# Performance work log

Measured on AMD Instinct MI355X. Metric: run time of the kernel, lower is better.

## Reference

```python
import jax, jax.numpy as jnp
import numpy as np

# graph structure constants (uniform graphs => simple coloring / masks all-true)
G, NV, EPG, LEPG = 128, 32, 64, 256          # graphs, nodes/graph, g-edges/graph, lg-edges/graph
NG, NLG, ELG, K = G * NV, G * EPG, G * LEPG, EPG  # K = n_colors = lg-nodes per graph
H, HF, T, L, NC, FIN, FE, NB = 32, 128, 8, 4, 12, 16, 16, 4  # hidden, hidden_final, towers, layers, classes, node feats, edge feats, basis

_FLOATS = ('x_g','edge_attr_g','x_lg','edge_attr_lg','W_enc','b_enc','W_msg','b_msg','W_init','b_init','np_l1_w','np_l1_b','np_l2_w','np_l2_b','np_lin_w','np_lin_b','fe_l1_w','fe_l1_b','fe_l2_w','fe_l2_b','fe_lin_w','fe_lin_b','gd_w','gd_b','ga_w','ga_b','ld_w','ld_b','la_w','la_b','u1_w','u1_b','u2_w','u2_b','u3_w','u3_b','en_w','en_b','li_w','li_b','lj_w','lj_b','bn_g','bn_b','ac_w','ac_b','fl_w','fl_b')

def _lin(x, w, b):
    return x @ w + b

def _glin(x, w, b):
    # grouped (tower) linear: w [T, c, c], block-diagonal over channel groups
    t, ci, co = w.shape
    y = jnp.einsum('...tc,tcd->...td', x.reshape(x.shape[:-1] + (t, ci)), w)
    return y.reshape(x.shape[:-1] + (t * co,)) + b

def setup_inputs():
    rng = np.random.default_rng(0)
    off_n = np.arange(G)[:, None] * NV
    ei_g = np.stack([(rng.integers(0, NV, (G, EPG)) + off_n).ravel(),
                     (rng.integers(0, NV, (G, EPG)) + off_n).ravel()])
    off_e = np.arange(G)[:, None] * EPG
    ei_lg = np.stack([(rng.integers(0, EPG, (G, LEPG)) + off_e).ravel(),
                      (rng.integers(0, EPG, (G, LEPG)) + off_e).ravel()])
    keys = iter(jax.random.split(jax.random.key(0), 64))
    def nrm(shape, fan):
        return (jax.random.normal(next(keys), shape, dtype=jnp.float32) / np.float32(np.sqrt(fan)))
    z = lambda *s: jnp.zeros(s, jnp.float32)
    inp = {
        'x_g': nrm((NG, FIN), 1.0),
        'edge_attr_g': nrm((NLG, FE), 1.0),
        'x_lg': nrm((NLG, NB), 1.0),
        'edge_attr_lg': nrm((ELG, NB), 1.0),
        'W_enc': nrm((FIN, H), FIN), 'b_enc': z(H),
        'W_msg': nrm((2 * H + FE + NB, HF), 2 * H + FE + NB), 'b_msg': z(HF),
        'W_init': nrm((HF + 1, H), HF + 1), 'b_init': z(H),
        'np_l1_w': nrm((HF + 1, HF), HF + 1), 'np_l1_b': z(HF),
        'np_l2_w': nrm((HF + 1, HF), HF + 1), 'np_l2_b': z(HF),
        'np_lin_w': nrm((HF, HF), HF), 'np_lin_b': z(HF),
        'fe_l1_w': nrm((H, HF), H), 'fe_l1_b': z(HF),
        'fe_l2_w': nrm((H, HF), H), 'fe_l2_b': z(HF),
        'fe_lin_w': nrm((HF, HF), HF), 'fe_lin_b': z(HF),
        'gd_w': nrm((NB, NB), NB), 'gd_b': z(NB),
        'ga_w': nrm((NB, NB), NB), 'ga_b': z(NB),
        'ld_w': nrm((L, NB, H), NB), 'ld_b': z(L, H),
        'la_w': nrm((L, NB, H), NB), 'la_b': z(L, H),
        'u1_w': nrm((L, T, H // T, H // T), H // T), 'u1_b': z(L, H),
        'u2_w': nrm((L, T, H // T, H // T), H // T), 'u2_b': z(L, H),
        'u3_w': nrm((L, T, H // T, H // T), H // T), 'u3_b': z(L, H),
        'en_w': nrm((L, H, H), H), 'en_b': z(L, H),
        'li_w': nrm((L, T, H // T, H // T), H // T), 'li_b': z(L, H),
        'lj_w': nrm((L, T, H // T, H // T), H // T), 'lj_b': z(L, H),
        'bn_g': jnp.ones((L, H), jnp.float32), 'bn_b': z(L, H),
        'ac_w': nrm((HF, HF), HF), 'ac_b': z(HF),
        'fl_w': nrm((HF, NC), HF), 'fl_b': z(NC),
        'edge_index_g': jnp.asarray(ei_g, dtype=jnp.int32),
        'edge_index_lg': jnp.asarray(ei_lg, dtype=jnp.int32),
        'batch_g': jnp.asarray(np.repeat(np.arange(G), NV), dtype=jnp.int32),
    }
    return inp

def _forward(fl, edge_index_g, edge_index_lg, batch_g):
    p = dict(zip(_FLOATS, fl))
    h = _lin(p['x_g'], p['W_enc'], p['b_enc'])                                 # [NG, H]
    s, d = edge_index_g[0], edge_index_g[1]
    hm = _lin(jnp.concatenate([h[s], h[d], p['edge_attr_g'], p['x_lg']], -1),
              p['W_msg'], p['b_msg'])                                          # [NLG, HF]
    batch_lg = batch_g[s]                                                      # graph id per lg node
    coloring = jnp.arange(NLG, dtype=jnp.int32) - batch_lg * EPG               # local color in [0, K)
    onehot = (coloring[:, None] == jnp.arange(K)).astype(hm.dtype)             # [NLG, K]
    # map_x_to_u: one-hot identity channel + features on own color row
    u = jnp.concatenate([onehot[:, :, None], onehot[:, :, None] * hm[:, None, :]], 2)  # [NLG, K, HF+1]
    edge_glob = _lin(p['edge_attr_lg'], p['ga_w'], p['ga_b'])                  # [ELG, NB]
    dist_glob = _lin(p['x_lg'], p['gd_w'], p['gd_b'])                          # [NLG, NB]
    ls, ld = edge_index_lg[0], edge_index_lg[1]
    indeg = jax.ops.segment_sum(jnp.ones((ELG,), hm.dtype), ld, num_segments=NLG)
    avg_e = (jax.ops.segment_sum(indeg, batch_lg, num_segments=G) / EPG)[batch_lg]  # avg edges/graph per node
    idx = jnp.arange(NLG)
    nb = jnp.asarray(EPG, hm.dtype)                                            # lg nodes per graph

    def extract(u, w1, b1, w2, b2, lw, lb):
        # GraphExtractor: UtoGlobal (mean-over-colors pool + diagonal pool) + residual relu lin
        mean = jax.ops.segment_sum(u.sum(1) / nb, batch_lg, num_segments=G) / nb
        diag = jax.ops.segment_sum(u[idx, coloring], batch_lg, num_segments=G) / nb
        out = _lin(mean, w1, b1) + _lin(diag, w2, b2)
        return out + jax.nn.relu(_lin(out, lw, lb))

    out = extract(u, p['np_l1_w'], p['np_l1_b'], p['np_l2_w'], p['np_l2_b'], p['np_lin_w'], p['np_lin_b'])
    u = _lin(u, p['W_init'], p['b_init'])                                      # [NLG, K, H]
    for i in range(L):
        if i > 0:  # batch norm (training-mode stats over nodes x colors)
            m = u.mean((0, 1)); v = u.var((0, 1))
            u = (u - m) * jax.lax.rsqrt(v + 1e-5) * p['bn_g'][i] + p['bn_b'][i]
        dist_loc = _lin(dist_glob, p['ld_w'][i], p['ld_b'][i])                 # [NLG, H]
        edge_loc = _lin(edge_glob, p['la_w'][i], p['la_b'][i])                 # [ELG, H]
        # SMPLayer: UtoU message net (entrywise + color-mean + diagonal terms, towered)
        um = (_glin(u, p['u1_w'][i], p['u1_b'][i])
              + _glin(u.sum(1) / nb, p['u2_w'][i], p['u2_b'][i])[:, None, :]
              + _glin(u[idx, coloring], p['u3_w'][i], p['u3_b'][i])[:, None, :])
        um = um * dist_loc[:, None, :]                                         # distance-basis filter
        ui = _glin(um, p['li_w'][i], p['li_b'][i])
        uj = _glin(um, p['lj_w'][i], p['lj_b'][i])
        ef = _lin(edge_loc, p['en_w'][i], p['en_b'][i])[:, None, :]
        msg = um[ls] + jax.nn.relu(ui[ld] + uj[ls] + ef)                       # [ELG, K, H]
        u = jax.ops.segment_sum(msg, ld, num_segments=NLG) / avg_e[:, None, None] + u
        out = out + extract(u, p['fe_l1_w'], p['fe_l1_b'], p['fe_l2_w'], p['fe_l2_b'], p['fe_lin_w'], p['fe_lin_b']) / L
    out = jax.nn.relu(_lin(out, p['ac_w'], p['ac_b'])) + out
    return _lin(out, p['fl_w'], p['fl_b'])                                     # [G, NC]

def reference(x_g, edge_attr_g, x_lg, edge_attr_lg, W_enc, b_enc, W_msg, b_msg, W_init, b_init, np_l1_w, np_l1_b, np_l2_w, np_l2_b, np_lin_w, np_lin_b, fe_l1_w, fe_l1_b, fe_l2_w, fe_l2_b, fe_lin_w, fe_lin_b, gd_w, gd_b, ga_w, ga_b, ld_w, ld_b, la_w, la_b, u1_w, u1_b, u2_w, u2_b, u3_w, u3_b, en_w, en_b, li_w, li_b, lj_w, lj_b, bn_g, bn_b, ac_w, ac_b, fl_w, fl_b, edge_index_g, edge_index_lg, batch_g):
    args = dict(locals())
    fl = tuple(args[n] for n in _FLOATS)
    return _forward(fl, edge_index_g, edge_index_lg, batch_g)
```

## Files before the change

### kernel.cpp

```cpp
#include <hip/hip_runtime.h>

#define G_    128
#define NV_   32
#define EPG_  64
#define LEPG_ 256
#define NG_   (G_*NV_)
#define NLG_  (G_*EPG_)
#define ELG_  (G_*LEPG_)
#define K_    64
#define H_    32
#define HF_   128
#define L_    4
#define NC_   12
#define FIN_  16
#define FE_   16
#define NB_   4
#define TILE_ (K_*H_)

__global__ void k_init(float* bna) {
    int t = threadIdx.x;
    if (t < 256) bna[t] = 0.f;
}

__global__ __launch_bounds__(256) void k_pre(
    const float* __restrict__ xg, const float* __restrict__ Wenc,
    const float* __restrict__ benc,
    const float* __restrict__ ealg, const float* __restrict__ gaw,
    const float* __restrict__ gab,
    const float* __restrict__ xlg, const float* __restrict__ gdw,
    const float* __restrict__ gdb,
    float* __restrict__ h, float* __restrict__ eglob, float* __restrict__ dglob)
{
    int bid = blockIdx.x, t = threadIdx.x;
    if (bid < 512) {
        int gid = bid*256 + t; int nn = gid>>5, ch = gid&31;
        float s = benc[ch];
#pragma unroll
        for (int f = 0; f < FIN_; ++f) s += xg[nn*FIN_+f]*Wenc[f*H_+ch];
        h[gid] = s;
    } else {
        int gid = (bid-512)*256 + t;
        if (gid < ELG_*4) {
            int e = gid>>2, k = gid&3;
            float s = gab[k];
#pragma unroll
            for (int j = 0; j < 4; ++j) s += ealg[e*4+j]*gaw[j*4+k];
            eglob[gid] = s;
        } else {
            int gid2 = gid - ELG_*4;
            int nn = gid2>>2, k = gid2&3;
            float s = gdb[k];
#pragma unroll
            for (int j = 0; j < 4; ++j) s += xlg[nn*4+j]*gdw[j*4+k];
            dglob[gid2] = s;
        }
    }
}

__global__ __launch_bounds__(256) void k_p12(
    const float* __restrict__ h, const float* __restrict__ Wm,
    float* __restrict__ p1, float* __restrict__ p2) {
    int bid = blockIdx.x, t = threadIdx.x;
    int n = bid*2 + (t>>7), o = t&127;
    const float* hn = h + n*32;
    float a = 0.f, b = 0.f;
#pragma unroll
    for (int k = 0; k < 32; ++k) {
        float hv = hn[k];
        a += hv * Wm[k*HF_ + o];
        b += hv * Wm[(32+k)*HF_ + o];
    }
    p1[n*HF_ + o] = a; p2[n*HF_ + o] = b;
}

__global__ __launch_bounds__(256) void k_q34(
    const float* __restrict__ eag, const float* __restrict__ xlg,
    const float* __restrict__ Wm, const float* __restrict__ bm,
    float* __restrict__ q34) {
    int bid = blockIdx.x, t = threadIdx.x;
    int e = bid*2 + (t>>7), o = t&127;
    float s = bm[o];
#pragma unroll
    for (int k = 0; k < 16; ++k) s += eag[e*16+k] * Wm[(64+k)*HF_ + o];
#pragma unroll
    for (int k = 0; k < 4; ++k)  s += xlg[e*4+k]  * Wm[(80+k)*HF_ + o];
    q34[e*HF_ + o] = s;
}

__global__ __launch_bounds__(256) void k_msg2(
    const float* __restrict__ p1, const float* __restrict__ p2,
    const float* __restrict__ q34, const int* __restrict__ sidx,
    const int* __restrict__ didx, float* __restrict__ hm) {
    int idx = blockIdx.x*256 + threadIdx.x;
    int e = idx >> 5, o4 = idx & 31;
    int s = sidx[e], d = didx[e];
    float4 a = ((const float4*)p1)[s*32 + o4];
    float4 b = ((const float4*)p2)[d*32 + o4];
    float4 q = ((const float4*)q34)[e*32 + o4];
    ((float4*)hm)[idx] = make_float4(a.x+b.x+q.x, a.y+b.y+q.y, a.z+b.z+q.z, a.w+b.w+q.w);
}

__global__ __launch_bounds__(128) void k_out0(
    const float* __restrict__ hm, const float* __restrict__ l1w,
    const float* __restrict__ l1b, const float* __restrict__ l2w,
    const float* __restrict__ l2b, const float* __restrict__ lnw,
    const float* __restrict__ lnb, float* __restrict__ out_acc) {
    __shared__ float mh[128], o1[128];
    int g = blockIdx.x, t = threadIdx.x;
    float s = 0.f;
    for (int k = 0; k < 64; ++k) s += hm[(g*64+k)*HF_ + t];
    mh[t] = s * (1.f/64.f);
    __syncthreads();
    float o = l1b[t] + l2b[t] + (l1w[t]*(1.f/64.f) + l2w[t]);
    for (int k = 0; k < 128; ++k)
        o += mh[k] * (l1w[(1+k)*HF_ + t]*(1.f/64.f) + l2w[(1+k)*HF_ + t]);
    o1[t] = o;
    __syncthreads();
    float r = lnb[t];
    for (int k = 0; k < 128; ++k) r += o1[k] * lnw[k*HF_ + t];
    out_acc[g*HF_ + t] = o + (r > 0.f ? r : 0.f);
}

__global__ __launch_bounds__(256) void k_rv(
    const float* __restrict__ hm, const float* __restrict__ Wi,
    const float* __restrict__ bi, float* __restrict__ rv,
    float* __restrict__ cs, float* __restrict__ ds) {
    int bid = blockIdx.x, t = threadIdx.x;
    int n = bid*8 + (t>>5), ch = t&31;
    float s = Wi[ch];
    for (int f = 0; f < HF_; ++f) s += hm[n*HF_ + f] * Wi[(1+f)*H_ + ch];
    rv[n*32 + ch] = s;
    cs[n*32 + ch] = 64.f*bi[ch] + s;
    ds[n*32 + ch] = bi[ch] + s;
}

__global__ __launch_bounds__(256) void k_u0w(
    const float* __restrict__ rv, const float* __restrict__ bi,
    float* __restrict__ u0) {
    int bid = blockIdx.x, t = threadIdx.x;
    int c4 = t & 7;
    float4 b4 = ((const float4*)bi)[c4];
#pragma unroll
    for (int k = 0; k < 8; ++k) {
        int lin = bid*2048 + k*256 + t;
        int n = lin >> 9, c = (lin >> 3) & 63;
        float4 v = b4;
        if (c == (n & 63)) {
            float4 r = ((const float4*)rv)[n*8 + c4];
            v.x += r.x; v.y += r.y; v.z += r.z; v.w += r.w;
        }
        ((float4*)u0)[lin] = v;
    }
}

__global__ __launch_bounds__(256) void k_csr(
    const int* __restrict__ ls, const int* __restrict__ ld,
    int* __restrict__ offsg, int* __restrict__ csrp) {
    __shared__ int cnt[64], offs[65], cur[64];
    int g = blockIdx.x, t = threadIdx.x;
    if (t < 64) cnt[t] = 0;
    __syncthreads();
    int d = 0, sl = 0;
    d = ld[g*256 + t] & 63;
    sl = ls[g*256 + t] & 63;
    atomicAdd(&cnt[d], 1);
    __syncthreads();
    if (t == 0) {
        int a = 0;
        for (int i = 0; i < 64; ++i) { offs[i] = a; a += cnt[i]; }
        offs[64] = a;
    }
    __syncthreads();
    if (t < 64) { cur[t] = offs[t]; offsg[g*65 + t] = offs[t]; }
    if (t == 0) offsg[g*65 + 64] = offs[64];
    __syncthreads();
    int p = atomicAdd(&cur[d], 1);
    csrp[g*256 + p] = (t << 6) | sl;
}

__global__ __launch_bounds__(256) void k_dlef(
    const float* __restrict__ dgl, const float* __restrict__ egl,
    const float* __restrict__ ldw, const float* __restrict__ ldb,
    const float* __restrict__ law, const float* __restrict__ lab,
    const float* __restrict__ enw, const float* __restrict__ enb,
    float* __restrict__ dlb, float* __restrict__ efb) {
    int bid = blockIdx.x, t = threadIdx.x;
    if (bid < 4096) {
        int gid = bid*256 + t;
        int l = gid >> 18, rem = gid & ((1<<18)-1);
        int n = rem >> 5, ch = rem & 31;
        float s = ldb[l*32 + ch];
#pragma unroll
        for (int j = 0; j < 4; ++j) s += dgl[n*4+j] * ldw[l*128 + j*32 + ch];
        dlb[gid] = s;
    } else {
        __shared__ float el[8][32];
        int p = (bid - 4096)*8 + (t >> 5);
        int ch = t & 31;
        int l = p >> 15, e = p & 32767;
        float s = lab[l*32 + ch];
#pragma unroll
        for (int j = 0; j < 4; ++j) s += egl[e*4+j] * law[l*128 + j*32 + ch];
        el[t>>5][ch] = s;
        __syncthreads();
        float o = enb[l*32 + ch];
        for (int k = 0; k < 32; ++k) o += el[t>>5][k] * enw[l*1024 + k*32 + ch];
        efb[(size_t)l*ELG_*32 + e*32 + ch] = o;
    }
}

__global__ __launch_bounds__(256) void k_gtdl(
    const float* __restrict__ cs, const float* __restrict__ ds,
    const float* __restrict__ bnaP, const float* __restrict__ bng,
    const float* __restrict__ bnb, int lay,
    const float* __restrict__ u1w, const float* __restrict__ u2w,
    const float* __restrict__ u3w, const float* __restrict__ u1b,
    const float* __restrict__ u2b, const float* __restrict__ u3b,
    const float* __restrict__ dl_l, float* __restrict__ gtb) {
    int idx = blockIdx.x*256 + threadIdx.x;
    int n = idx >> 5, ch = idx & 31;
    int chi = ch & 3, twb = ch & ~3;
    float gt = u1b[ch] + u2b[ch] + u3b[ch];
#pragma unroll
    for (int j = 0; j < 4; ++j) {
        int bj = twb + j;
        float s_ = 1.f, sh_ = 0.f;
        if (lay > 0) {
            float m = bnaP[bj] * (1.f/524288.f);
            float v = bnaP[32+bj] * (1.f/524288.f) - m*m;
            s_ = bng[bj] * rsqrtf(v + 1e-5f);
            sh_ = bnb[bj] - m*s_;
        }
        float csF = s_*cs[n*32 + bj] + 64.f*sh_;
        float dgF = s_*ds[n*32 + bj] + sh_;
        gt += csF*(1.f/64.f)*u2w[bj*4 + chi] + dgF*u3w[bj*4 + chi]
            + sh_*u1w[bj*4 + chi];
    }
    gtb[idx] = gt * dl_l[idx];
}

#define PROC_NODE(ACC, UI, JE)                                              \
  for (; j < (JE); ++j) {                                                   \
    int jn = j + 2; jn = jn < 255 ? jn : 255;                               \
    int pkN = ep[jn];                                                       \
    float4 efN = *(const float4*)(ef_l + (((size_t)((g<<8)+(pkN>>6)))<<5) + chb); \
    int src = pkA & 63;                                                     \
    float4 u4 = *(float4*)&um[src*128 + coff];                              \
    float r0 = UI.x + efA.x + blj4[0] + u4.x*wj[0] + u4.y*wj[4] + u4.z*wj[8] + u4.w*wj[12]; \
    float r1 = UI.y + efA.y + blj4[1] + u4.x*wj[1] + u4.y*wj[5] + u4.z*wj[9] + u4.w*wj[13]; \
    float r2 = UI.z + efA.z + blj4[2] + u4.x*wj[2] + u4.y*wj[6] + u4.z*wj[10] + u4.w*wj[14]; \
    float r3 = UI.w + efA.w + blj4[3] + u4.x*wj[3] + u4.y*wj[7] + u4.z*wj[11] + u4.w*wj[15]; \
    ACC.x += u4.x + (r0>0.f?r0:0.f);                                        \
    ACC.y += u4.y + (r1>0.f?r1:0.f);                                        \
    ACC.z += u4.z + (r2>0.f?r2:0.f);                                        \
    ACC.w += u4.w + (r3>0.f?r3:0.f);                                        \
    pkA = pkB; efA = efB; pkB = pkN; efB = efN;                             \
  }

#define UM_NODE(I, UIOUT, DL, GT)                                           \
  {                                                                         \
    int nl = nq*4 + I;                                                      \
    float4 uv = *(float4*)&us[nl*128 + coff];                               \
    float m0 = (uv.x*w1f[0]+uv.y*w1f[4]+uv.z*w1f[8] +uv.w*w1f[12])*DL.x + GT.x; \
    float m1 = (uv.x*w1f[1]+uv.y*w1f[5]+uv.z*w1f[9] +uv.w*w1f[13])*DL.y + GT.y; \
    float m2 = (uv.x*w1f[2]+uv.y*w1f[6]+uv.z*w1f[10]+uv.w*w1f[14])*DL.z + GT.z; \
    float m3 = (uv.x*w1f[3]+uv.y*w1f[7]+uv.z*w1f[11]+uv.w*w1f[15])*DL.w + GT.w; \
    *(float4*)&um[nl*128 + coff] = make_float4(m0,m1,m2,m3);                \
    UIOUT.x = bli4[0] + m0*wi[0] + m1*wi[4] + m2*wi[8]  + m3*wi[12];        \
    UIOUT.y = bli4[1] + m0*wi[1] + m1*wi[5] + m2*wi[9]  + m3*wi[13];        \
    UIOUT.z = bli4[2] + m0*wi[2] + m1*wi[6] + m2*wi[10] + m3*wi[14];        \
    UIOUT.w = bli4[3] + m0*wi[3] + m1*wi[7] + m2*wi[11] + m3*wi[15];        \
  }

#define UN_NODE(I, ACC)                                                     \
  {                                                                         \
    float4 uo4 = *(float4*)&us[(nq*4+I)*128 + coff];                        \
    float4 un4;                                                             \
    un4.x = ACC.x*0.25f + sc4[0]*uo4.x + sh4[0];                            \
    un4.y = ACC.y*0.25f + sc4[1]*uo4.y + sh4[1];                            \
    un4.z = ACC.z*0.25f + sc4[2]*uo4.z + sh4[2];                            \
    un4.w = ACC.w*0.25f + sc4[3]*uo4.w + sh4[3];                            \
    *(float4*)(u_out + (((size_t)(n0g+I))<<11) + (ck<<7) + coff) = un4;     \
    if (nq == ck && c == I)                                                 \
        *(float4*)&dsb[(((size_t)(n0g+I))<<5) + chb] = un4;                 \
    float cx=un4.x, cy=un4.y, cz=un4.z, cw=un4.w;                           \
    float qx=cx*cx, qy=cy*cy, qz=cz*cz, qw=cw*cw;                           \
    cx+=__shfl_xor(cx,8);  cy+=__shfl_xor(cy,8);  cz+=__shfl_xor(cz,8);  cw+=__shfl_xor(cw,8); \
    qx+=__shfl_xor(qx,8);  qy+=__shfl_xor(qy,8);  qz+=__shfl_xor(qz,8);  qw+=__shfl_xor(qw,8); \
    cx+=__shfl_xor(cx,16); cy+=__shfl_xor(cy,16); cz+=__shfl_xor(cz,16); cw+=__shfl_xor(cw,16); \
    qx+=__shfl_xor(qx,16); qy+=__shfl_xor(qy,16); qz+=__shfl_xor(qz,16); qw+=__shfl_xor(qw,16); \
    if (c == 0) {                                                           \
        *(float4*)&pcs[(((size_t)(ck*NLG_ + n0g + I))<<5) + chb] = make_float4(cx,cy,cz,cw); \
        *(float4*)&pss[(((size_t)(ck*NLG_ + n0g + I))<<5) + chb] = make_float4(qx,qy,qz,qw); \
    }                                                                       \
  }

__global__ __launch_bounds__(512, 4) void k_layer(
    const float* __restrict__ u_in, float* __restrict__ u_out,
    const int* __restrict__ offsg, const int* __restrict__ csrp,
    const float* __restrict__ bnaP, const float* __restrict__ bng,
    const float* __restrict__ bnb, int lay,
    const float* __restrict__ u1w,
    const float* __restrict__ liw, const float* __restrict__ lib,
    const float* __restrict__ ljw, const float* __restrict__ ljb,
    const float* __restrict__ dl_l, const float* __restrict__ gtb,
    const float* __restrict__ ef_l,
    float* __restrict__ pcs, float* __restrict__ pss, float* __restrict__ dsb)
{
    __shared__ float us[64*128];
    __shared__ float um[64*128];
    __shared__ int ep[256];
    __shared__ int offs[65];

    const int bid = blockIdx.x, t = threadIdx.x;
    const int g  = ((bid >> 7) << 3) | (bid & 7);
    const int ck = (bid >> 3) & 15;
    const int tw = t & 7, c = (t >> 3) & 3, nq = t >> 5;
    const int chb = tw * 4;
    const int coff = c*32 + chb;
    const int n0g = g*64 + nq*4;

    if (t < 256) ep[t] = csrp[g*256 + t];
    else if (t < 256 + 65) offs[t - 256] = offsg[g*65 + (t - 256)];

    {
        const float* ub = u_in + ((size_t)g << 17) + (ck << 7);
#pragma unroll
        for (int r = 0; r < 4; ++r) {
            int lin = r*2048 + t*4;
            int nl = lin >> 7, off = lin & 127;
            float4 v = *(const float4*)(ub + ((size_t)nl << 11) + off);
            *(float4*)&us[lin] = v;
        }
    }

    float4 dl0 = *(const float4*)(dl_l + (((size_t)(n0g+0))<<5) + chb);
    float4 dl1 = *(const float4*)(dl_l + (((size_t)(n0g+1))<<5) + chb);
    float4 dl2 = *(const float4*)(dl_l + (((size_t)(n0g+2))<<5) + chb);
    float4 dl3 = *(const float4*)(dl_l + (((size_t)(n0g+3))<<5) + chb);
    float4 gt0 = *(const float4*)(gtb + (((size_t)(n0g+0))<<5) + chb);
    float4 gt1 = *(const float4*)(gtb + (((size_t)(n0g+1))<<5) + chb);
    float4 gt2 = *(const float4*)(gtb + (((size_t)(n0g+2))<<5) + chb);
    float4 gt3 = *(const float4*)(gtb + (((size_t)(n0g+3))<<5) + chb);

    float sc4[4], sh4[4];
    if (lay > 0) {
#pragma unroll
        for (int j = 0; j < 4; ++j) {
            int bj = chb + j;
            float m = bnaP[bj] * (1.f/524288.f);
            float v = bnaP[32+bj] * (1.f/524288.f) - m*m;
            float s_ = bng[bj] * rsqrtf(v + 1e-5f);
            sc4[j] = s_; sh4[j] = bnb[bj] - m*s_;
        }
    } else {
#pragma unroll
        for (int j = 0; j < 4; ++j) { sc4[j] = 1.f; sh4[j] = 0.f; }
    }
    float w1f[16], wi[16], wj[16], bli4[4], blj4[4];
#pragma unroll
    for (int j = 0; j < 4; ++j)
#pragma unroll
        for (int d = 0; d < 4; ++d) {
            w1f[j*4+d] = u1w[(chb+j)*4 + d] * sc4[j];
            wi [j*4+d] = liw[(chb+j)*4 + d];
            wj [j*4+d] = ljw[(chb+j)*4 + d];
        }
#pragma unroll
    for (int d = 0; d < 4; ++d) { bli4[d] = lib[chb+d]; blj4[d] = ljb[chb+d]; }

    __syncthreads();

    float4 ui0, ui1, ui2, ui3;
    UM_NODE(0, ui0, dl0, gt0)
    UM_NODE(1, ui1, dl1, gt1)
    UM_NODE(2, ui2, dl2, gt2)
    UM_NODE(3, ui3, dl3, gt3)
    __syncthreads();

    float4 acc0 = make_float4(0,0,0,0), acc1 = acc0, acc2 = acc0, acc3 = acc0;
    int j = offs[nq*4];
    {
        int ja = j < 255 ? j : 255;
        int pkA = ep[ja];
        float4 efA = *(const float4*)(ef_l + (((size_t)((g<<8)+(pkA>>6)))<<5) + chb);
        int jb = (j+1) < 255 ? (j+1) : 255;
        int pkB = ep[jb];
        float4 efB = *(const float4*)(ef_l + (((size_t)((g<<8)+(pkB>>6)))<<5) + chb);
        int e1 = offs[nq*4+1], e2 = offs[nq*4+2], e3 = offs[nq*4+3], e4 = offs[nq*4+4];
        PROC_NODE(acc0, ui0, e1)
        PROC_NODE(acc1, ui1, e2)
        PROC_NODE(acc2, ui2, e3)
        PROC_NODE(acc3, ui3, e4)
    }

    UN_NODE(0, acc0)
    UN_NODE(1, acc1)
    UN_NODE(2, acc2)
    UN_NODE(3, acc3)
}

__global__ __launch_bounds__(256) void k_midx(
    const float* __restrict__ pcs, const float* __restrict__ pss,
    const float* __restrict__ dsb,
    const float* __restrict__ l1w, const float* __restrict__ l1b,
    const float* __restrict__ l2w, const float* __restrict__ l2b,
    const float* __restrict__ lnw, const float* __restrict__ lnb,
    float* __restrict__ csb, float* __restrict__ bna_i,
    float* __restrict__ out_acc, float scale)
{
    __shared__ float red[3*128];
    __shared__ float S[32], D[32], o1[128];
    int g = blockIdx.x, t = threadIdx.x;
    int ch = t & 31, ng = t >> 5;
    float pS = 0.f, pQ = 0.f, pD = 0.f;
#pragma unroll
    for (int k = 0; k < 8; ++k) {
        int n = g*64 + ng + 8*k;
        float cs_ = 0.f, ss_ = 0.f;
#pragma unroll
        for (int ckk = 0; ckk < 16; ++ckk) {
            cs_ += pcs[((size_t)ckk*NLG_ + n)*32 + ch];
            ss_ += pss[((size_t)ckk*NLG_ + n)*32 + ch];
        }
        csb[n*32 + ch] = cs_;
        pS += cs_; pQ += ss_;
        pD += dsb[n*32 + ch];
    }
    pS += __shfl_xor(pS, 32); pQ += __shfl_xor(pQ, 32); pD += __shfl_xor(pD, 32);
    int w = t >> 6;
    if ((t & 63) < 32) {
        red[w*32 + ch] = pS;
        red[128 + w*32 + ch] = pQ;
        red[256 + w*32 + ch] = pD;
    }
    __syncthreads();
    if (t < 32) {
        float S_ = 0.f, Q_ = 0.f, D_ = 0.f;
#pragma unroll
        for (int ww = 0; ww < 4; ++ww) {
            S_ += red[ww*32 + t]; Q_ += red[128 + ww*32 + t]; D_ += red[256 + ww*32 + t];
        }
        S[t] = S_; D[t] = D_;
        atomicAdd(&bna_i[t], S_);
        atomicAdd(&bna_i[32 + t], Q_);
    }
    __syncthreads();
    float o = 0.f;
    if (t < 128) {
        o = l1b[t] + l2b[t];
        for (int k = 0; k < 32; ++k)
            o += (S[k]*(1.f/4096.f))*l1w[k*HF_ + t] + (D[k]*(1.f/64.f))*l2w[k*HF_ + t];
        o1[t] = o;
    }
    __syncthreads();
    if (t < 128) {
        float r = lnb[t];
        for (int k = 0; k < 128; ++k) r += o1[k] * lnw[k*HF_ + t];
        out_acc[g*HF_ + t] += (o + (r > 0.f ? r : 0.f)) * scale;
    }
}

__global__ __launch_bounds__(128) void k_final(
    const float* __restrict__ out_acc, const float* __restrict__ acw,
    const float* __restrict__ acb, const float* __restrict__ flw,
    const float* __restrict__ flb, float* __restrict__ out) {
    __shared__ float t1[128];
    int g = blockIdx.x, t = threadIdx.x;
    float o = out_acc[g*HF_ + t];
    float r = acb[t];
    for (int k = 0; k < 128; ++k) r += out_acc[g*HF_ + k] * acw[k*HF_ + t];
    t1[t] = o + (r > 0.f ? r : 0.f);
    __syncthreads();
    if (t < NC_) {
        float s = flb[t];
        for (int k = 0; k < 128; ++k) s += t1[k] * flw[k*NC_ + t];
        out[g*NC_ + t] = s;
    }
}

extern "C" void kernel_launch(void* const* d_in, const int* in_sizes, int n_in,
                              void* d_out, int out_size, void* d_ws, size_t ws_size,
                              hipStream_t stream) {
    const float* x_g      = (const float*)d_in[0];
    const float* eag      = (const float*)d_in[1];
    const float* x_lg     = (const float*)d_in[2];
    const float* ealg     = (const float*)d_in[3];
    const float* W_enc    = (const float*)d_in[4];
    const float* b_enc    = (const float*)d_in[5];
    const float* W_msg    = (const float*)d_in[6];
    const float* b_msg    = (const float*)d_in[7];
    const float* W_init   = (const float*)d_in[8];
    const float* b_init   = (const float*)d_in[9];
    const float* np_l1_w  = (const float*)d_in[10];
    const float* np_l1_b  = (const float*)d_in[11];
    const float* np_l2_w  = (const float*)d_in[12];
    const float* np_l2_b  = (const float*)d_in[13];
    const float* np_lin_w = (const float*)d_in[14];
    const float* np_lin_b = (const float*)d_in[15];
    const float* fe_l1_w  = (const float*)d_in[16];
    const float* fe_l1_b  = (const float*)d_in[17];
    const float* fe_l2_w  = (const float*)d_in[18];
    const float* fe_l2_b  = (const float*)d_in[19];
    const float* fe_lin_w = (const float*)d_in[20];
    const float* fe_lin_b = (const float*)d_in[21];
    const float* gd_w     = (const float*)d_in[22];
    const float* gd_b     = (const float*)d_in[23];
    const float* ga_w     = (const float*)d_in[24];
    const float* ga_b     = (const float*)d_in[25];
    const float* ld_w     = (const float*)d_in[26];
    const float* ld_b     = (const float*)d_in[27];
    const float* la_w     = (const float*)d_in[28];
    const float* la_b     = (const float*)d_in[29];
    const float* u1_w     = (const float*)d_in[30];
    const float* u1_b     = (const float*)d_in[31];
    const float* u2_w     = (const float*)d_in[32];
    const float* u2_b     = (const float*)d_in[33];
    const float* u3_w     = (const float*)d_in[34];
    const float* u3_b     = (const float*)d_in[35];
    const float* en_w     = (const float*)d_in[36];
    const float* en_b     = (const float*)d_in[37];
    const float* li_w     = (const float*)d_in[38];
    const float* li_b     = (const float*)d_in[39];
    const float* lj_w     = (const float*)d_in[40];
    const float* lj_b     = (const float*)d_in[41];
    const float* bn_g     = (const float*)d_in[42];
    const float* bn_b     = (const float*)d_in[43];
    const float* ac_w     = (const float*)d_in[44];
    const float* ac_b     = (const float*)d_in[45];
    const float* fl_w     = (const float*)d_in[46];
    const float* fl_b     = (const float*)d_in[47];
    const int*   ei_g     = (const int*)d_in[48];
    const int*   ei_lg    = (const int*)d_in[49];

    const int* s_g  = ei_g;
    const int* d_g  = ei_g + NLG_;
    const int* ls   = ei_lg;
    const int* ldst = ei_lg + ELG_;

    float* ws = (float*)d_ws;
    size_t o = 0;
    float* ub0  = ws + o; o += (size_t)NLG_ * TILE_;
    float* ub1  = ws + o; o += (size_t)NLG_ * TILE_;
    float* hm   = ws + o; o += (size_t)NLG_ * HF_;
    float* hbuf = ws + o; o += (size_t)NG_ * H_;
    float* dgl  = ws + o; o += (size_t)NLG_ * NB_;
    float* egl  = ws + o; o += (size_t)ELG_ * NB_;
    float* p1b  = ws + o; o += (size_t)NG_ * HF_;
    float* p2b  = ws + o; o += (size_t)NG_ * HF_;
    float* q34b = ws + o; o += (size_t)NLG_ * HF_;
    float* rvb  = ws + o; o += (size_t)NLG_ * 32;
    float* csb  = ws + o; o += (size_t)NLG_ * 32;
    float* dsb  = ws + o; o += (size_t)NLG_ * 32;
    float* gtb  = ws + o; o += (size_t)NLG_ * 32;
    float* pcs  = ws + o; o += (size_t)16 * NLG_ * 32;
    float* pss  = ws + o; o += (size_t)16 * NLG_ * 32;
    float* oac  = ws + o; o += (size_t)G_ * HF_;
    float* bna  = ws + o; o += 256;
    float* dlb  = ws + o; o += (size_t)L_ * NLG_ * 32;
    float* efb  = ws + o; o += (size_t)L_ * ELG_ * 32;
    int*   offsg = (int*)(ws + o); o += G_ * 65;
    int*   csrp  = (int*)(ws + o); o += ELG_;

    k_init<<<1, 256, 0, stream>>>(bna);
    k_pre<<<1152, 256, 0, stream>>>(x_g, W_enc, b_enc, ealg, ga_w, ga_b,
                                    x_lg, gd_w, gd_b, hbuf, egl, dgl);
    k_p12<<<2048, 256, 0, stream>>>(hbuf, W_msg, p1b, p2b);
    k_q34<<<4096, 256, 0, stream>>>(eag, x_lg, W_msg, b_msg, q34b);
    k_msg2<<<1024, 256, 0, stream>>>(p1b, p2b, q34b, s_g, d_g, hm);
    k_dlef<<<4096 + 16384, 256, 0, stream>>>(dgl, egl, ld_w, ld_b, la_w, la_b,
                                             en_w, en_b, dlb, efb);
    k_out0<<<G_, 128, 0, stream>>>(hm, np_l1_w, np_l1_b, np_l2_w, np_l2_b,
                                   np_lin_w, np_lin_b, oac);
    k_rv<<<1024, 256, 0, stream>>>(hm, W_init, b_init, rvb, csb, dsb);
    k_u0w<<<2048, 256, 0, stream>>>(rvb, b_init, ub0);
    k_csr<<<G_, 256, 0, stream>>>(ls, ldst, offsg, csrp);
    k_gtdl<<<1024, 256, 0, stream>>>(csb, dsb, bna, bn_g, bn_b, 0,
                                     u1_w, u2_w, u3_w, u1_b, u2_b, u3_b,
                                     dlb, gtb);

    float* ubufs[2] = {ub0, ub1};
    for (int i = 0; i < L_; ++i) {
        const float* ui = ubufs[i & 1];
        float* uo = ubufs[(i + 1) & 1];
        k_layer<<<2048, 512, 0, stream>>>(
            ui, uo, offsg, csrp,
            (i > 0 ? bna + (i-1)*64 : bna), bn_g + i*32, bn_b + i*32, i,
            u1_w + i*128,
            li_w + i*128, li_b + i*32,
            lj_w + i*128, lj_b + i*32,
            dlb + (size_t)i*NLG_*32, gtb, efb + (size_t)i*ELG_*32,
            pcs, pss, dsb);
        k_midx<<<G_, 256, 0, stream>>>(
            pcs, pss, dsb,
            fe_l1_w, fe_l1_b, fe_l2_w, fe_l2_b, fe_lin_w, fe_lin_b,
            csb, bna + i*64, oac, 1.0f / (float)L_);
        if (i < L_ - 1)
            k_gtdl<<<1024, 256, 0, stream>>>(csb, dsb, bna + i*64,
                                             bn_g + (i+1)*32, bn_b + (i+1)*32, i+1,
                                             u1_w + (i+1)*128, u2_w + (i+1)*128,
                                             u3_w + (i+1)*128, u1_b + (i+1)*32,
                                             u2_b + (i+1)*32, u3_b + (i+1)*32,
                                             dlb + (size_t)(i+1)*NLG_*32, gtb);
    }
    k_final<<<G_, 128, 0, stream>>>(oac, ac_w, ac_b, fl_w, fl_b, (float*)d_out);
}
```

Before: 571.5 us.

## Merge preprocessing kernels, drop u shared staging, synthesize layer-0 u, fuse final head

```diff
diff --git a/kernel.cpp b/kernel.cpp
--- a/kernel.cpp
+++ b/kernel.cpp
@@ -17,176 +17,134 @@
 #define NB_   4
 #define TILE_ (K_*H_)
 
-__global__ void k_init(float* bna) {
-    int t = threadIdx.x;
-    if (t < 256) bna[t] = 0.f;
-}
-
-__global__ __launch_bounds__(256) void k_pre(
+__global__ __launch_bounds__(256) void kA(
     const float* __restrict__ xg, const float* __restrict__ Wenc,
     const float* __restrict__ benc,
     const float* __restrict__ ealg, const float* __restrict__ gaw,
     const float* __restrict__ gab,
     const float* __restrict__ xlg, const float* __restrict__ gdw,
     const float* __restrict__ gdb,
-    float* __restrict__ h, float* __restrict__ eglob, float* __restrict__ dglob)
+    const float* __restrict__ eag, const float* __restrict__ Wm,
+    const float* __restrict__ bm,
+    const float* __restrict__ h_unused,
+    const int* __restrict__ ls, const int* __restrict__ ldst,
+    float* __restrict__ h, float* __restrict__ eglob, float* __restrict__ dglob,
+    float* __restrict__ p1, float* __restrict__ p2, float* __restrict__ q34,
+    int* __restrict__ offsg, int* __restrict__ csrp, float* __restrict__ bna)
 {
+    __shared__ int cnt[64], offs[65], cur[64];
     int bid = blockIdx.x, t = threadIdx.x;
-    if (bid < 512) {
-        int gid = bid*256 + t; int nn = gid>>5, ch = gid&31;
-        float s = benc[ch];
-#pragma unroll
-        for (int f = 0; f < FIN_; ++f) s += xg[nn*FIN_+f]*Wenc[f*H_+ch];
-        h[gid] = s;
-    } else {
-        int gid = (bid-512)*256 + t;
-        if (gid < ELG_*4) {
-            int e = gid>>2, k = gid&3;
-            float s = gab[k];
-#pragma unroll
-            for (int j = 0; j < 4; ++j) s += ealg[e*4+j]*gaw[j*4+k];
-            eglob[gid] = s;
+    if (bid == 0) {
+        bna[t] = 0.f;
+        return;
+    }
+    if (bid < 1 + 1152) {
+        int lb = bid - 1;
+        if (lb < 512) {
+            int gid = lb*256 + t; int nn = gid>>5, ch = gid&31;
+            float s = benc[ch];
+#pragma unroll
+            for (int f = 0; f < FIN_; ++f) s += xg[nn*FIN_+f]*Wenc[f*H_+ch];
+            h[gid] = s;
         } else {
-            int gid2 = gid - ELG_*4;
-            int nn = gid2>>2, k = gid2&3;
-            float s = gdb[k];
-#pragma unroll
-            for (int j = 0; j < 4; ++j) s += xlg[nn*4+j]*gdw[j*4+k];
-            dglob[gid2] = s;
-        }
+            int gid = (lb-512)*256 + t;
+            if (gid < ELG_*4) {
+                int e = gid>>2, k = gid&3;
+                float s = gab[k];
+#pragma unroll
+                for (int j = 0; j < 4; ++j) s += ealg[e*4+j]*gaw[j*4+k];
+                eglob[gid] = s;
+            } else {
+                int gid2 = gid - ELG_*4;
+                int nn = gid2>>2, k = gid2&3;
+                float s = gdb[k];
+#pragma unroll
+                for (int j = 0; j < 4; ++j) s += xlg[nn*4+j]*gdw[j*4+k];
+                dglob[gid2] = s;
+            }
+        }
+        return;
+    }
+    if (bid < 1 + 1152 + 2048) {
+        int lb = bid - 1153;
+        int n = lb*2 + (t>>7), o = t&127;
+        const float* hn = h_unused + n*32;
+        (void)hn;
+        float hv[32];
+#pragma unroll
+        for (int k = 0; k < 32; ++k) {
+            float s = benc[k];
+#pragma unroll
+            for (int f = 0; f < FIN_; ++f) s += xg[n*FIN_+f]*Wenc[f*H_+k];
+            hv[k] = s;
+        }
+        float a = 0.f, b = 0.f;
+#pragma unroll
+        for (int k = 0; k < 32; ++k) {
+            a += hv[k] * Wm[k*HF_ + o];
+            b += hv[k] * Wm[(32+k)*HF_ + o];
+        }
+        p1[n*HF_ + o] = a; p2[n*HF_ + o] = b;
+        return;
+    }
+    if (bid < 1 + 1152 + 2048 + 4096) {
+        int lb = bid - 3201;
+        int e = lb*2 + (t>>7), o = t&127;
+        float s = bm[o];
+#pragma unroll
+        for (int k = 0; k < 16; ++k) s += eag[e*16+k] * Wm[(64+k)*HF_ + o];
+#pragma unroll
+        for (int k = 0; k < 4; ++k)  s += xlg[e*4+k]  * Wm[(80+k)*HF_ + o];
+        q34[e*HF_ + o] = s;
+        return;
+    }
+    {
+        int g = bid - 7297;
+        if (t < 64) cnt[t] = 0;
+        __syncthreads();
+        int d = ldst[g*256 + t] & 63;
+        int sl = ls[g*256 + t] & 63;
+        atomicAdd(&cnt[d], 1);
+        __syncthreads();
+        if (t == 0) {
+            int a = 0;
+            for (int i = 0; i < 64; ++i) { offs[i] = a; a += cnt[i]; }
+            offs[64] = a;
+        }
+        __syncthreads();
+        if (t < 64) { cur[t] = offs[t]; offsg[g*65 + t] = offs[t]; }
+        if (t == 0) offsg[g*65 + 64] = offs[64];
+        __syncthreads();
+        int p = atomicAdd(&cur[d], 1);
+        csrp[g*256 + p] = (t << 6) | sl;
     }
 }
 
-__global__ __launch_bounds__(256) void k_p12(
-    const float* __restrict__ h, const float* __restrict__ Wm,
-    float* __restrict__ p1, float* __restrict__ p2) {
-    int bid = blockIdx.x, t = threadIdx.x;
-    int n = bid*2 + (t>>7), o = t&127;
-    const float* hn = h + n*32;
-    float a = 0.f, b = 0.f;
-#pragma unroll
-    for (int k = 0; k < 32; ++k) {
-        float hv = hn[k];
-        a += hv * Wm[k*HF_ + o];
-        b += hv * Wm[(32+k)*HF_ + o];
-    }
-    p1[n*HF_ + o] = a; p2[n*HF_ + o] = b;
-}
-
-__global__ __launch_bounds__(256) void k_q34(
-    const float* __restrict__ eag, const float* __restrict__ xlg,
-    const float* __restrict__ Wm, const float* __restrict__ bm,
-    float* __restrict__ q34) {
-    int bid = blockIdx.x, t = threadIdx.x;
-    int e = bid*2 + (t>>7), o = t&127;
-    float s = bm[o];
-#pragma unroll
-    for (int k = 0; k < 16; ++k) s += eag[e*16+k] * Wm[(64+k)*HF_ + o];
-#pragma unroll
-    for (int k = 0; k < 4; ++k)  s += xlg[e*4+k]  * Wm[(80+k)*HF_ + o];
-    q34[e*HF_ + o] = s;
-}
-
-__global__ __launch_bounds__(256) void k_msg2(
+__global__ __launch_bounds__(256) void kB(
     const float* __restrict__ p1, const float* __restrict__ p2,
     const float* __restrict__ q34, const int* __restrict__ sidx,
-    const int* __restrict__ didx, float* __restrict__ hm) {
-    int idx = blockIdx.x*256 + threadIdx.x;
-    int e = idx >> 5, o4 = idx & 31;
-    int s = sidx[e], d = didx[e];
-    float4 a = ((const float4*)p1)[s*32 + o4];
-    float4 b = ((const float4*)p2)[d*32 + o4];
-    float4 q = ((const float4*)q34)[e*32 + o4];
-    ((float4*)hm)[idx] = make_float4(a.x+b.x+q.x, a.y+b.y+q.y, a.z+b.z+q.z, a.w+b.w+q.w);
-}
-
-__global__ __launch_bounds__(128) void k_out0(
-    const float* __restrict__ hm, const float* __restrict__ l1w,
-    const float* __restrict__ l1b, const float* __restrict__ l2w,
-    const float* __restrict__ l2b, const float* __restrict__ lnw,
-    const float* __restrict__ lnb, float* __restrict__ out_acc) {
-    __shared__ float mh[128], o1[128];
-    int g = blockIdx.x, t = threadIdx.x;
-    float s = 0.f;
-    for (int k = 0; k < 64; ++k) s += hm[(g*64+k)*HF_ + t];
-    mh[t] = s * (1.f/64.f);
-    __syncthreads();
-    float o = l1b[t] + l2b[t] + (l1w[t]*(1.f/64.f) + l2w[t]);
-    for (int k = 0; k < 128; ++k)
-        o += mh[k] * (l1w[(1+k)*HF_ + t]*(1.f/64.f) + l2w[(1+k)*HF_ + t]);
-    o1[t] = o;
-    __syncthreads();
-    float r = lnb[t];
-    for (int k = 0; k < 128; ++k) r += o1[k] * lnw[k*HF_ + t];
-    out_acc[g*HF_ + t] = o + (r > 0.f ? r : 0.f);
-}
-
-__global__ __launch_bounds__(256) void k_rv(
-    const float* __restrict__ hm, const float* __restrict__ Wi,
-    const float* __restrict__ bi, float* __restrict__ rv,
-    float* __restrict__ cs, float* __restrict__ ds) {
-    int bid = blockIdx.x, t = threadIdx.x;
-    int n = bid*8 + (t>>5), ch = t&31;
-    float s = Wi[ch];
-    for (int f = 0; f < HF_; ++f) s += hm[n*HF_ + f] * Wi[(1+f)*H_ + ch];
-    rv[n*32 + ch] = s;
-    cs[n*32 + ch] = 64.f*bi[ch] + s;
-    ds[n*32 + ch] = bi[ch] + s;
-}
-
-__global__ __launch_bounds__(256) void k_u0w(
-    const float* __restrict__ rv, const float* __restrict__ bi,
-    float* __restrict__ u0) {
-    int bid = blockIdx.x, t = threadIdx.x;
-    int c4 = t & 7;
-    float4 b4 = ((const float4*)bi)[c4];
-#pragma unroll
-    for (int k = 0; k < 8; ++k) {
-        int lin = bid*2048 + k*256 + t;
-        int n = lin >> 9, c = (lin >> 3) & 63;
-        float4 v = b4;
-        if (c == (n & 63)) {
-            float4 r = ((const float4*)rv)[n*8 + c4];
-            v.x += r.x; v.y += r.y; v.z += r.z; v.w += r.w;
-        }
-        ((float4*)u0)[lin] = v;
-    }
-}
-
-__global__ __launch_bounds__(256) void k_csr(
-    const int* __restrict__ ls, const int* __restrict__ ld,
-    int* __restrict__ offsg, int* __restrict__ csrp) {
-    __shared__ int cnt[64], offs[65], cur[64];
-    int g = blockIdx.x, t = threadIdx.x;
-    if (t < 64) cnt[t] = 0;
-    __syncthreads();
-    int d = 0, sl = 0;
-    d = ld[g*256 + t] & 63;
-    sl = ls[g*256 + t] & 63;
-    atomicAdd(&cnt[d], 1);
-    __syncthreads();
-    if (t == 0) {
-        int a = 0;
-        for (int i = 0; i < 64; ++i) { offs[i] = a; a += cnt[i]; }
-        offs[64] = a;
-    }
-    __syncthreads();
-    if (t < 64) { cur[t] = offs[t]; offsg[g*65 + t] = offs[t]; }
-    if (t == 0) offsg[g*65 + 64] = offs[64];
-    __syncthreads();
-    int p = atomicAdd(&cur[d], 1);
-    csrp[g*256 + p] = (t << 6) | sl;
-}
-
-__global__ __launch_bounds__(256) void k_dlef(
+    const int* __restrict__ didx, float* __restrict__ hm,
     const float* __restrict__ dgl, const float* __restrict__ egl,
     const float* __restrict__ ldw, const float* __restrict__ ldb,
     const float* __restrict__ law, const float* __restrict__ lab,
     const float* __restrict__ enw, const float* __restrict__ enb,
-    float* __restrict__ dlb, float* __restrict__ efb) {
+    float* __restrict__ dlb, float* __restrict__ efb)
+{
+    __shared__ float el[8][32];
     int bid = blockIdx.x, t = threadIdx.x;
-    if (bid < 4096) {
-        int gid = bid*256 + t;
+    if (bid < 1024) {
+        int idx = bid*256 + t;
+        int e = idx >> 5, o4 = idx & 31;
+        int s = sidx[e], d = didx[e];
+        float4 a = ((const float4*)p1)[s*32 + o4];
+        float4 b = ((const float4*)p2)[d*32 + o4];
+        float4 q = ((const float4*)q34)[e*32 + o4];
+        ((float4*)hm)[idx] = make_float4(a.x+b.x+q.x, a.y+b.y+q.y, a.z+b.z+q.z, a.w+b.w+q.w);
+        return;
+    }
+    int lb = bid - 1024;
+    if (lb < 4096) {
+        int gid = lb*256 + t;
         int l = gid >> 18, rem = gid & ((1<<18)-1);
         int n = rem >> 5, ch = rem & 31;
         float s = ldb[l*32 + ch];
@@ -194,8 +152,7 @@
         for (int j = 0; j < 4; ++j) s += dgl[n*4+j] * ldw[l*128 + j*32 + ch];
         dlb[gid] = s;
     } else {
-        __shared__ float el[8][32];
-        int p = (bid - 4096)*8 + (t >> 5);
+        int p = (lb - 4096)*8 + (t >> 5);
         int ch = t & 31;
         int l = p >> 15, e = p & 32767;
         float s = lab[l*32 + ch];
@@ -206,6 +163,48 @@
         float o = enb[l*32 + ch];
         for (int k = 0; k < 32; ++k) o += el[t>>5][k] * enw[l*1024 + k*32 + ch];
         efb[(size_t)l*ELG_*32 + e*32 + ch] = o;
+    }
+}
+
+__global__ __launch_bounds__(256) void kC(
+    const float* __restrict__ hm, const float* __restrict__ Wi,
+    const float* __restrict__ bi, float* __restrict__ rv,
+    float* __restrict__ cs, float* __restrict__ ds,
+    const float* __restrict__ l1w, const float* __restrict__ l1b,
+    const float* __restrict__ l2w, const float* __restrict__ l2b,
+    const float* __restrict__ lnw, const float* __restrict__ lnb,
+    float* __restrict__ out_acc)
+{
+    __shared__ float mh[128], o1[128];
+    int bid = blockIdx.x, t = threadIdx.x;
+    if (bid < 1024) {
+        int n = bid*8 + (t>>5), ch = t&31;
+        float s = Wi[ch];
+        for (int f = 0; f < HF_; ++f) s += hm[n*HF_ + f] * Wi[(1+f)*H_ + ch];
+        rv[n*32 + ch] = s;
+        cs[n*32 + ch] = 64.f*bi[ch] + s;
+        ds[n*32 + ch] = bi[ch] + s;
+        return;
+    }
+    int g = bid - 1024;
+    if (t < 128) {
+        float s = 0.f;
+        for (int k = 0; k < 64; ++k) s += hm[(g*64+k)*HF_ + t];
+        mh[t] = s * (1.f/64.f);
+    }
+    __syncthreads();
+    float o = 0.f;
+    if (t < 128) {
+        o = l1b[t] + l2b[t] + (l1w[t]*(1.f/64.f) + l2w[t]);
+        for (int k = 0; k < 128; ++k)
+            o += mh[k] * (l1w[(1+k)*HF_ + t]*(1.f/64.f) + l2w[(1+k)*HF_ + t]);
+        o1[t] = o;
+    }
+    __syncthreads();
+    if (t < 128) {
+        float r = lnb[t];
+        for (int k = 0; k < 128; ++k) r += o1[k] * lnw[k*HF_ + t];
+        out_acc[g*HF_ + t] = o + (r > 0.f ? r : 0.f);
     }
 }
 
@@ -257,30 +256,28 @@
     pkA = pkB; efA = efB; pkB = pkN; efB = efN;                             \
   }
 
-#define UM_NODE(I, UIOUT, DL, GT)                                           \
+#define UM_NODE(I, UIOUT, UO, DL, GT)                                       \
   {                                                                         \
-    int nl = nq*4 + I;                                                      \
-    float4 uv = *(float4*)&us[nl*128 + coff];                               \
-    float m0 = (uv.x*w1f[0]+uv.y*w1f[4]+uv.z*w1f[8] +uv.w*w1f[12])*DL.x + GT.x; \
-    float m1 = (uv.x*w1f[1]+uv.y*w1f[5]+uv.z*w1f[9] +uv.w*w1f[13])*DL.y + GT.y; \
-    float m2 = (uv.x*w1f[2]+uv.y*w1f[6]+uv.z*w1f[10]+uv.w*w1f[14])*DL.z + GT.z; \
-    float m3 = (uv.x*w1f[3]+uv.y*w1f[7]+uv.z*w1f[11]+uv.w*w1f[15])*DL.w + GT.w; \
-    *(float4*)&um[nl*128 + coff] = make_float4(m0,m1,m2,m3);                \
+    float m0 = (UO.x*w1f[0]+UO.y*w1f[4]+UO.z*w1f[8] +UO.w*w1f[12])*DL.x + GT.x; \
+    float m1 = (UO.x*w1f[1]+UO.y*w1f[5]+UO.z*w1f[9] +UO.w*w1f[13])*DL.y + GT.y; \
+    float m2 = (UO.x*w1f[2]+UO.y*w1f[6]+UO.z*w1f[10]+UO.w*w1f[14])*DL.z + GT.z; \
+    float m3 = (UO.x*w1f[3]+UO.y*w1f[7]+UO.z*w1f[11]+UO.w*w1f[15])*DL.w + GT.w; \
+    *(float4*)&um[(nq*4+I)*128 + coff] = make_float4(m0,m1,m2,m3);          \
     UIOUT.x = bli4[0] + m0*wi[0] + m1*wi[4] + m2*wi[8]  + m3*wi[12];        \
     UIOUT.y = bli4[1] + m0*wi[1] + m1*wi[5] + m2*wi[9]  + m3*wi[13];        \
     UIOUT.z = bli4[2] + m0*wi[2] + m1*wi[6] + m2*wi[10] + m3*wi[14];        \
     UIOUT.w = bli4[3] + m0*wi[3] + m1*wi[7] + m2*wi[11] + m3*wi[15];        \
   }
 
-#define UN_NODE(I, ACC)                                                     \
+#define UN_NODE(I, ACC, UO)                                                 \
   {                                                                         \
-    float4 uo4 = *(float4*)&us[(nq*4+I)*128 + coff];                        \
     float4 un4;                                                             \
-    un4.x = ACC.x*0.25f + sc4[0]*uo4.x + sh4[0];                            \
-    un4.y = ACC.y*0.25f + sc4[1]*uo4.y + sh4[1];                            \
-    un4.z = ACC.z*0.25f + sc4[2]*uo4.z + sh4[2];                            \
-    un4.w = ACC.w*0.25f + sc4[3]*uo4.w + sh4[3];                            \
-    *(float4*)(u_out + (((size_t)(n0g+I))<<11) + (ck<<7) + coff) = un4;     \
+    un4.x = ACC.x*0.25f + sc4[0]*UO.x + sh4[0];                             \
+    un4.y = ACC.y*0.25f + sc4[1]*UO.y + sh4[1];                             \
+    un4.z = ACC.z*0.25f + sc4[2]*UO.z + sh4[2];                             \
+    un4.w = ACC.w*0.25f + sc4[3]*UO.w + sh4[3];                             \
+    if (!last)                                                              \
+        *(float4*)(u_out + (((size_t)(n0g+I))<<11) + (ck<<7) + coff) = un4; \
     if (nq == ck && c == I)                                                 \
         *(float4*)&dsb[(((size_t)(n0g+I))<<5) + chb] = un4;                 \
     float cx=un4.x, cy=un4.y, cz=un4.z, cw=un4.w;                           \
@@ -295,11 +292,12 @@
     }                                                                       \
   }
 
-__global__ __launch_bounds__(512, 4) void k_layer(
+__global__ __launch_bounds__(512, 6) void k_layer(
     const float* __restrict__ u_in, float* __restrict__ u_out,
     const int* __restrict__ offsg, const int* __restrict__ csrp,
     const float* __restrict__ bnaP, const float* __restrict__ bng,
-    const float* __restrict__ bnb, int lay,
+    const float* __restrict__ bnb, int lay, int last,
+    const float* __restrict__ rvb, const float* __restrict__ bi,
     const float* __restrict__ u1w,
     const float* __restrict__ liw, const float* __restrict__ lib,
     const float* __restrict__ ljw, const float* __restrict__ ljb,
@@ -307,7 +305,6 @@
     const float* __restrict__ ef_l,
     float* __restrict__ pcs, float* __restrict__ pss, float* __restrict__ dsb)
 {
-    __shared__ float us[64*128];
     __shared__ float um[64*128];
     __shared__ int ep[256];
     __shared__ int offs[65];
@@ -323,15 +320,23 @@
     if (t < 256) ep[t] = csrp[g*256 + t];
     else if (t < 256 + 65) offs[t - 256] = offsg[g*65 + (t - 256)];
 
-    {
-        const float* ub = u_in + ((size_t)g << 17) + (ck << 7);
-#pragma unroll
-        for (int r = 0; r < 4; ++r) {
-            int lin = r*2048 + t*4;
-            int nl = lin >> 7, off = lin & 127;
-            float4 v = *(const float4*)(ub + ((size_t)nl << 11) + off);
-            *(float4*)&us[lin] = v;
-        }
+    float4 uo0, uo1, uo2, uo3;
+    if (lay == 0) {
+        float4 b4 = *(const float4*)(bi + chb);
+        uo0 = b4; uo1 = b4; uo2 = b4; uo3 = b4;
+        if (nq == ck) {
+            float4 r = *(const float4*)(rvb + (size_t)(n0g + c)*32 + chb);
+            if      (c == 0) { uo0.x+=r.x; uo0.y+=r.y; uo0.z+=r.z; uo0.w+=r.w; }
+            else if (c == 1) { uo1.x+=r.x; uo1.y+=r.y; uo1.z+=r.z; uo1.w+=r.w; }
+            else if (c == 2) { uo2.x+=r.x; uo2.y+=r.y; uo2.z+=r.z; uo2.w+=r.w; }
+            else             { uo3.x+=r.x; uo3.y+=r.y; uo3.z+=r.z; uo3.w+=r.w; }
+        }
+    } else {
+        const float* ub = u_in + ((size_t)n0g << 11) + (ck << 7) + coff;
+        uo0 = *(const float4*)(ub);
+        uo1 = *(const float4*)(ub + 2048);
+        uo2 = *(const float4*)(ub + 4096);
+        uo3 = *(const float4*)(ub + 6144);
     }
 
     float4 dl0 = *(const float4*)(dl_l + (((size_t)(n0g+0))<<5) + chb);
@@ -346,36 +351,34 @@
     float sc4[4], sh4[4];
     if (lay > 0) {
 #pragma unroll
-        for (int j = 0; j < 4; ++j) {
-            int bj = chb + j;
+        for (int j2 = 0; j2 < 4; ++j2) {
+            int bj = chb + j2;
             float m = bnaP[bj] * (1.f/524288.f);
             float v = bnaP[32+bj] * (1.f/524288.f) - m*m;
             float s_ = bng[bj] * rsqrtf(v + 1e-5f);
-            sc4[j] = s_; sh4[j] = bnb[bj] - m*s_;
+            sc4[j2] = s_; sh4[j2] = bnb[bj] - m*s_;
         }
     } else {
 #pragma unroll
-        for (int j = 0; j < 4; ++j) { sc4[j] = 1.f; sh4[j] = 0.f; }
+        for (int j2 = 0; j2 < 4; ++j2) { sc4[j2] = 1.f; sh4[j2] = 0.f; }
     }
     float w1f[16], wi[16], wj[16], bli4[4], blj4[4];
 #pragma unroll
-    for (int j = 0; j < 4; ++j)
+    for (int j2 = 0; j2 < 4; ++j2)
 #pragma unroll
         for (int d = 0; d < 4; ++d) {
-            w1f[j*4+d] = u1w[(chb+j)*4 + d] * sc4[j];
-            wi [j*4+d] = liw[(chb+j)*4 + d];
-            wj [j*4+d] = ljw[(chb+j)*4 + d];
+            w1f[j2*4+d] = u1w[(chb+j2)*4 + d] * sc4[j2];
+            wi [j2*4+d] = liw[(chb+j2)*4 + d];
+            wj [j2*4+d] = ljw[(chb+j2)*4 + d];
         }
 #pragma unroll
     for (int d = 0; d < 4; ++d) { bli4[d] = lib[chb+d]; blj4[d] = ljb[chb+d]; }
 
-    __syncthreads();
-
     float4 ui0, ui1, ui2, ui3;
-    UM_NODE(0, ui0, dl0, gt0)
-    UM_NODE(1, ui1, dl1, gt1)
-    UM_NODE(2, ui2, dl2, gt2)
-    UM_NODE(3, ui3, dl3, gt3)
+    UM_NODE(0, ui0, uo0, dl0, gt0)
+    UM_NODE(1, ui1, uo1, dl1, gt1)
+    UM_NODE(2, ui2, uo2, dl2, gt2)
+    UM_NODE(3, ui3, uo3, dl3, gt3)
     __syncthreads();
 
     float4 acc0 = make_float4(0,0,0,0), acc1 = acc0, acc2 = acc0, acc3 = acc0;
@@ -394,10 +397,10 @@
         PROC_NODE(acc3, ui3, e4)
     }
 
-    UN_NODE(0, acc0)
-    UN_NODE(1, acc1)
-    UN_NODE(2, acc2)
-    UN_NODE(3, acc3)
+    UN_NODE(0, acc0, uo0)
+    UN_NODE(1, acc1, uo1)
+    UN_NODE(2, acc2, uo2)
+    UN_NODE(3, acc3, uo3)
 }
 
 __global__ __launch_bounds__(256) void k_midx(
@@ -407,10 +410,13 @@
     const float* __restrict__ l2w, const float* __restrict__ l2b,
     const float* __restrict__ lnw, const float* __restrict__ lnb,
     float* __restrict__ csb, float* __restrict__ bna_i,
-    float* __restrict__ out_acc, float scale)
+    float* __restrict__ out_acc, float scale,
+    int do_final, const float* __restrict__ acw, const float* __restrict__ acb,
+    const float* __restrict__ flw, const float* __restrict__ flb,
+    float* __restrict__ outp)
 {
     __shared__ float red[3*128];
-    __shared__ float S[32], D[32], o1[128];
+    __shared__ float S[32], D[32], o1[128], ov[128], t1[128];
     int g = blockIdx.x, t = threadIdx.x;
     int ch = t & 31, ng = t >> 5;
     float pS = 0.f, pQ = 0.f, pD = 0.f;
@@ -454,28 +460,27 @@
         o1[t] = o;
     }
     __syncthreads();
+    float newv = 0.f;
     if (t < 128) {
         float r = lnb[t];
         for (int k = 0; k < 128; ++k) r += o1[k] * lnw[k*HF_ + t];
-        out_acc[g*HF_ + t] += (o + (r > 0.f ? r : 0.f)) * scale;
-    }
-}
-
-__global__ __launch_bounds__(128) void k_final(
-    const float* __restrict__ out_acc, const float* __restrict__ acw,
-    const float* __restrict__ acb, const float* __restrict__ flw,
-    const float* __restrict__ flb, float* __restrict__ out) {
-    __shared__ float t1[128];
-    int g = blockIdx.x, t = threadIdx.x;
-    float o = out_acc[g*HF_ + t];
-    float r = acb[t];
-    for (int k = 0; k < 128; ++k) r += out_acc[g*HF_ + k] * acw[k*HF_ + t];
-    t1[t] = o + (r > 0.f ? r : 0.f);
-    __syncthreads();
-    if (t < NC_) {
-        float s = flb[t];
-        for (int k = 0; k < 128; ++k) s += t1[k] * flw[k*NC_ + t];
-        out[g*NC_ + t] = s;
+        newv = out_acc[g*HF_ + t] + (o + (r > 0.f ? r : 0.f)) * scale;
+        out_acc[g*HF_ + t] = newv;
+        ov[t] = newv;
+    }
+    if (do_final) {
+        __syncthreads();
+        if (t < 128) {
+            float r2 = acb[t];
+            for (int k = 0; k < 128; ++k) r2 += ov[k] * acw[k*HF_ + t];
+            t1[t] = ov[t] + (r2 > 0.f ? r2 : 0.f);
+        }
+        __syncthreads();
+        if (t < NC_) {
+            float s2 = flb[t];
+            for (int k = 0; k < 128; ++k) s2 += t1[k] * flw[k*NC_ + t];
+            outp[g*NC_ + t] = s2;
+        }
     }
 }
 
@@ -562,19 +567,17 @@
     int*   offsg = (int*)(ws + o); o += G_ * 65;
     int*   csrp  = (int*)(ws + o); o += ELG_;
 
-    k_init<<<1, 256, 0, stream>>>(bna);
-    k_pre<<<1152, 256, 0, stream>>>(x_g, W_enc, b_enc, ealg, ga_w, ga_b,
-                                    x_lg, gd_w, gd_b, hbuf, egl, dgl);
-    k_p12<<<2048, 256, 0, stream>>>(hbuf, W_msg, p1b, p2b);
-    k_q34<<<4096, 256, 0, stream>>>(eag, x_lg, W_msg, b_msg, q34b);
-    k_msg2<<<1024, 256, 0, stream>>>(p1b, p2b, q34b, s_g, d_g, hm);
-    k_dlef<<<4096 + 16384, 256, 0, stream>>>(dgl, egl, ld_w, ld_b, la_w, la_b,
-                                             en_w, en_b, dlb, efb);
-    k_out0<<<G_, 128, 0, stream>>>(hm, np_l1_w, np_l1_b, np_l2_w, np_l2_b,
-                                   np_lin_w, np_lin_b, oac);
-    k_rv<<<1024, 256, 0, stream>>>(hm, W_init, b_init, rvb, csb, dsb);
-    k_u0w<<<2048, 256, 0, stream>>>(rvb, b_init, ub0);
-    k_csr<<<G_, 256, 0, stream>>>(ls, ldst, offsg, csrp);
+    kA<<<7425, 256, 0, stream>>>(x_g, W_enc, b_enc, ealg, ga_w, ga_b,
+                                 x_lg, gd_w, gd_b, eag, W_msg, b_msg,
+                                 hbuf, ls, ldst,
+                                 hbuf, egl, dgl, p1b, p2b, q34b,
+                                 offsg, csrp, bna);
+    kB<<<21504, 256, 0, stream>>>(p1b, p2b, q34b, s_g, d_g, hm,
+                                  dgl, egl, ld_w, ld_b, la_w, la_b,
+                                  en_w, en_b, dlb, efb);
+    kC<<<1152, 256, 0, stream>>>(hm, W_init, b_init, rvb, csb, dsb,
+                                 np_l1_w, np_l1_b, np_l2_w, np_l2_b,
+                                 np_lin_w, np_lin_b, oac);
     k_gtdl<<<1024, 256, 0, stream>>>(csb, dsb, bna, bn_g, bn_b, 0,
                                      u1_w, u2_w, u3_w, u1_b, u2_b, u3_b,
                                      dlb, gtb);
@@ -586,6 +589,8 @@
         k_layer<<<2048, 512, 0, stream>>>(
             ui, uo, offsg, csrp,
             (i > 0 ? bna + (i-1)*64 : bna), bn_g + i*32, bn_b + i*32, i,
+            (i == L_ - 1) ? 1 : 0,
+            rvb, b_init,
             u1_w + i*128,
             li_w + i*128, li_b + i*32,
             lj_w + i*128, lj_b + i*32,
@@ -594,7 +599,8 @@
         k_midx<<<G_, 256, 0, stream>>>(
             pcs, pss, dsb,
             fe_l1_w, fe_l1_b, fe_l2_w, fe_l2_b, fe_lin_w, fe_lin_b,
-            csb, bna + i*64, oac, 1.0f / (float)L_);
+            csb, bna + i*64, oac, 1.0f / (float)L_,
+            (i == L_ - 1) ? 1 : 0, ac_w, ac_b, fl_w, fl_b, (float*)d_out);
         if (i < L_ - 1)
             k_gtdl<<<1024, 256, 0, stream>>>(csb, dsb, bna + i*64,
                                              bn_g + (i+1)*32, bn_b + (i+1)*32, i+1,
@@ -603,5 +609,4 @@
                                              u2_b + (i+1)*32, u3_b + (i+1)*32,
                                              dlb + (size_t)(i+1)*NLG_*32, gtb);
     }
-    k_final<<<G_, 128, 0, stream>>>(oac, ac_w, ac_b, fl_w, fl_b, (float*)d_out);
 }
```

New measurement: 1.065 ms. 86.4% more time.
